# Performance work log

Measured on AMD Instinct MI355X. Metric: run time of the kernel, lower is better.

## Reference

```python
import jax, jax.numpy as jnp
import numpy as np

B, T, F_IN = 32, 2000, 1024
GROUPS, NUM_VARS, VQ_DIM = 2, 320, 256
VAR_DIM = VQ_DIM // GROUPS  # 128
TAU = 2.0  # curr_temp = max_temp at step 0
EPS = 1e-7


def setup_inputs() -> dict:
    key = jax.random.key(0)
    k1, k2, k3, k4 = jax.random.split(key, 4)
    x = jax.random.normal(k1, (B, T, F_IN), jnp.float32)
    # nn.Linear: weight ~ N(0,1) per module init, bias zeros
    proj_w = jax.random.normal(k2, (GROUPS * NUM_VARS, F_IN), jnp.float32)
    proj_b = jnp.zeros((GROUPS * NUM_VARS,), jnp.float32)
    # nn.init.uniform_ on vars (leading singleton dim dropped)
    codebook = jax.random.uniform(k3, (GROUPS * NUM_VARS, VAR_DIM), jnp.float32)
    # pre-sampled standard Gumbel noise (training-path gumbel_softmax)
    u = jax.random.uniform(k4, (B * T, GROUPS * NUM_VARS), jnp.float32, 1e-6, 1.0 - 1e-6)
    gumbel = -jnp.log(-jnp.log(u))
    return {"x": x, "proj_w": proj_w, "proj_b": proj_b, "codebook": codebook, "gumbel": gumbel}


def reference(x, proj_w, proj_b, codebook, gumbel):
    bsz, tsz, fsz = x.shape
    bt = bsz * tsz
    logits = x.reshape(bt, fsz) @ proj_w.T + proj_b                 # [BT, G*V]
    lg = logits.reshape(bt, GROUPS, NUM_VARS)                       # [BT, G, V]

    # hard codes (argmax of raw logits) -> code perplexity
    k = jnp.argmax(lg, axis=-1)                                     # [BT, G]
    hard_x = jax.nn.one_hot(k, NUM_VARS, dtype=lg.dtype)            # [BT, G, V]
    hard_probs = hard_x.mean(axis=0)                                # [G, V]
    code_perplexity = jnp.exp(-jnp.sum(hard_probs * jnp.log(hard_probs + EPS), -1)).sum()

    avg_probs = jax.nn.softmax(lg, axis=-1).mean(axis=0)            # [G, V]
    prob_perplex = jnp.exp(-jnp.sum(avg_probs * jnp.log(avg_probs + EPS), -1)).sum()

    # training path: gumbel_softmax(tau, hard=True) with straight-through
    g = gumbel.reshape(bt, GROUPS, NUM_VARS)
    y_soft = jax.nn.softmax((lg + g) / TAU, axis=-1)                # [BT, G, V]
    y_hard = jax.nn.one_hot(jnp.argmax(y_soft, -1), NUM_VARS, dtype=y_soft.dtype)
    y = y_hard + y_soft - jax.lax.stop_gradient(y_soft)             # straight-through

    # codebook weighted sum; original does (one_hot[...,None] * vars).sum over V
    cb = codebook.reshape(GROUPS, NUM_VARS, VAR_DIM)
    q = jnp.einsum("tgv,gvd->tgd", y, cb)                           # [BT, G, var_dim]
    q = q.reshape(bsz, tsz, VQ_DIM)
    return q, code_perplexity, prob_perplex
```

## Files before the change

kernel.cpp:

```cpp
#include <hip/hip_runtime.h>
#include <cstdint>
#include <cstddef>

#define BT_TOT 64000
#define FIN    1024
#define GV     640
#define NV     320
#define VD     128
#define INV_BT (1.0f/64000.0f)

#define ITER_B  81920
#define BUF_B   40960

typedef __attribute__((ext_vector_type(8))) __bf16 bf16x8;
typedef __attribute__((ext_vector_type(16))) float f32x16;

typedef __attribute__((address_space(1))) void gvoid_t;
typedef __attribute__((address_space(3))) void lvoid_t;

__device__ inline short f2bf(float x) {
    unsigned int u = __float_as_uint(x);
    unsigned int r = (u + 0x7fffu + ((u >> 16) & 1u)) >> 16;
    return (short)r;
}
__device__ inline float bf2f(short h) {
    return __uint_as_float(((unsigned int)(unsigned short)h) << 16);
}
__device__ inline bf16x8 ld_frag(const char* p) {
    union { uint4 u; bf16x8 v; } t;
    t.u = *(const uint4*)p;
    return t.v;
}
__device__ __forceinline__ void glds16(const void* g, void* l) {
    __builtin_amdgcn_global_load_lds((gvoid_t*)g, (lvoid_t*)l, 16, 0, 0);
}
__device__ __forceinline__ void cvt8(const float4 f0, const float4 f1,
                                     bf16x8& hh, bf16x8& ll) {
    union { float4 f[2]; float s[8]; } ua; ua.f[0] = f0; ua.f[1] = f1;
    union { short s[8]; bf16x8 v; } uh, ul;
#pragma unroll
    for (int e = 0; e < 8; ++e) {
        const short hb = f2bf(ua.s[e]);
        uh.s[e] = hb;
        ul.s[e] = f2bf(ua.s[e] - bf2f(hb));
    }
    hh = uh.v; ll = ul.v;
}

__global__ __launch_bounds__(256) void prep(
    const float* __restrict__ W, char* __restrict__ Wpk,
    float* __restrict__ psum_g, int* __restrict__ cnt_g)
{
    const int t = blockIdx.x * 256 + threadIdx.x;
    if (t < GV) { psum_g[t] = 0.f; cnt_g[t] = 0; }
    const int r    = t >> 7;
    const int ck8  = t & 127;
    const int iter = ck8 >> 2;
    const int c    = (ck8 >> 1) & 1;
    const int ch   = ck8 & 1;
    const int g    = (r >= NV) ? 1 : 0;
    const int cv   = r - g * NV;
    const float* src = W + (size_t)r * FIN + (size_t)ck8 * 8;
    const float4 a = ((const float4*)src)[0];
    const float4 b = ((const float4*)src)[1];
    float xs[8] = {a.x, a.y, a.z, a.w, b.x, b.y, b.z, b.w};
    short hi[8], lo[8];
#pragma unroll
    for (int e = 0; e < 8; ++e) {
        hi[e] = f2bf(xs[e]);
        lo[e] = f2bf(xs[e] - bf2f(hi[e]));
    }
    char* dst = Wpk + (size_t)iter * ITER_B + (size_t)g * BUF_B + (size_t)c * 20480
                    + (size_t)(cv * 32 + ch * 16);
    *(uint4*)dst           = *(uint4*)hi;
    *(uint4*)(dst + 10240) = *(uint4*)lo;
}

__global__ __launch_bounds__(512) void fused(
    const float* __restrict__ X, const char* __restrict__ Wpk,
    const float* __restrict__ bias, const float* __restrict__ gumbel,
    const float* __restrict__ codebook, float* __restrict__ q,
    float* __restrict__ psum_g, int* __restrict__ cnt_g)
{
    __shared__ __align__(16) char smem[2 * BUF_B];

    const int id = blockIdx.x;
    const int linear = (id & 7) * 64 + (id >> 3);
    if (linear >= 500) return;
    const int rb = linear >> 1, g = linear & 1;

    const int tid  = threadIdx.x;
    const int lane = tid & 63, wave = tid >> 6;
    const int cl = lane & 31, h = lane >> 5;
    const int row0 = rb * 256;
    const int arow = wave * 32 + cl;
    const int rdo  = cl * 32 + h * 16;

    f32x16 acc[10];
#pragma unroll
    for (int nt = 0; nt < 10; ++nt) acc[nt] = (f32x16)0.0f;

    const float* aptr  = X + (size_t)(row0 + arow) * FIN + h * 8;
    const char*  wbase = Wpk + (size_t)g * BUF_B;

    float4 xa0, xa1, xa2, xa3;
    {
#pragma unroll
        for (int j = 0; j < 5; ++j)
            glds16(wbase + (size_t)(tid + 512 * j) * 16, smem + (tid + 512 * j) * 16);
        __builtin_amdgcn_sched_barrier(0);
        xa0 = *(const float4*)(aptr);
        xa1 = *(const float4*)(aptr + 4);
        xa2 = *(const float4*)(aptr + 16);
        xa3 = *(const float4*)(aptr + 20);
        asm volatile("s_waitcnt vmcnt(4)" ::: "memory");
        __builtin_amdgcn_s_barrier();
    }

    for (int i = 0; i < 32; ++i) {
        const char* bufc = smem + (i & 1) * BUF_B;
        char* bufn = smem + ((i + 1) & 1) * BUF_B;
        const char* wsrc = wbase + (size_t)(i + 1) * ITER_B;
        const float* apn = aptr + (i + 1) * 32;
        const bool more = (i < 31);
        bf16x8 bh[5], bl[5], ah, al;

#pragma unroll
        for (int n = 0; n < 5; ++n) {
            bh[n] = ld_frag(bufc + n * 1024 + rdo);
            bl[n] = ld_frag(bufc + 10240 + n * 1024 + rdo);
        }
        if (more) {
            glds16(wsrc + (size_t)tid * 16,         bufn + tid * 16);
            glds16(wsrc + (size_t)(tid + 512) * 16, bufn + (tid + 512) * 16);
        }
        cvt8(xa0, xa1, ah, al);
        __builtin_amdgcn_sched_barrier(0);
        __builtin_amdgcn_s_barrier();
        asm volatile("s_waitcnt lgkmcnt(0)" ::: "memory");
        __builtin_amdgcn_sched_barrier(0);
        __builtin_amdgcn_s_setprio(1);
#pragma unroll
        for (int n = 0; n < 5; ++n) {
            acc[n] = __builtin_amdgcn_mfma_f32_32x32x16_bf16(ah, bh[n], acc[n], 0, 0, 0);
            acc[n] = __builtin_amdgcn_mfma_f32_32x32x16_bf16(al, bh[n], acc[n], 0, 0, 0);
            acc[n] = __builtin_amdgcn_mfma_f32_32x32x16_bf16(ah, bl[n], acc[n], 0, 0, 0);
        }
        __builtin_amdgcn_s_setprio(0);
        __builtin_amdgcn_s_barrier();

#pragma unroll
        for (int n = 0; n < 5; ++n) {
            bh[n] = ld_frag(bufc + (n + 5) * 1024 + rdo);
            bl[n] = ld_frag(bufc + 10240 + (n + 5) * 1024 + rdo);
        }
        if (more)
            glds16(wsrc + (size_t)(tid + 1024) * 16, bufn + (tid + 1024) * 16);
        __builtin_amdgcn_sched_barrier(0);
        __builtin_amdgcn_s_barrier();
        asm volatile("s_waitcnt lgkmcnt(0)" ::: "memory");
        __builtin_amdgcn_sched_barrier(0);
        __builtin_amdgcn_s_setprio(1);
#pragma unroll
        for (int n = 0; n < 5; ++n) {
            acc[n + 5] = __builtin_amdgcn_mfma_f32_32x32x16_bf16(ah, bh[n], acc[n + 5], 0, 0, 0);
            acc[n + 5] = __builtin_amdgcn_mfma_f32_32x32x16_bf16(al, bh[n], acc[n + 5], 0, 0, 0);
            acc[n + 5] = __builtin_amdgcn_mfma_f32_32x32x16_bf16(ah, bl[n], acc[n + 5], 0, 0, 0);
        }
        __builtin_amdgcn_s_setprio(0);
        __builtin_amdgcn_s_barrier();

#pragma unroll
        for (int n = 0; n < 5; ++n) {
            bh[n] = ld_frag(bufc + 20480 + n * 1024 + rdo);
            bl[n] = ld_frag(bufc + 30720 + n * 1024 + rdo);
        }
        if (more) {
            glds16(wsrc + (size_t)(tid + 1536) * 16, bufn + (tid + 1536) * 16);
            __builtin_amdgcn_sched_barrier(0);
            xa0 = *(const float4*)(apn);
            xa1 = *(const float4*)(apn + 4);
        }
        cvt8(xa2, xa3, ah, al);
        __builtin_amdgcn_sched_barrier(0);
        __builtin_amdgcn_s_barrier();
        asm volatile("s_waitcnt lgkmcnt(0)" ::: "memory");
        __builtin_amdgcn_sched_barrier(0);
        __builtin_amdgcn_s_setprio(1);
#pragma unroll
        for (int n = 0; n < 5; ++n) {
            acc[n] = __builtin_amdgcn_mfma_f32_32x32x16_bf16(ah, bh[n], acc[n], 0, 0, 0);
            acc[n] = __builtin_amdgcn_mfma_f32_32x32x16_bf16(al, bh[n], acc[n], 0, 0, 0);
            acc[n] = __builtin_amdgcn_mfma_f32_32x32x16_bf16(ah, bl[n], acc[n], 0, 0, 0);
        }
        __builtin_amdgcn_s_setprio(0);
        __builtin_amdgcn_s_barrier();

#pragma unroll
        for (int n = 0; n < 5; ++n) {
            bh[n] = ld_frag(bufc + 20480 + (n + 5) * 1024 + rdo);
            bl[n] = ld_frag(bufc + 30720 + (n + 5) * 1024 + rdo);
        }
        if (more) {
            glds16(wsrc + (size_t)(tid + 2048) * 16, bufn + (tid + 2048) * 16);
            __builtin_amdgcn_sched_barrier(0);
            xa2 = *(const float4*)(apn + 16);
            xa3 = *(const float4*)(apn + 20);
        }
        __builtin_amdgcn_sched_barrier(0);
        __builtin_amdgcn_s_barrier();
        asm volatile("s_waitcnt lgkmcnt(0)" ::: "memory");
        __builtin_amdgcn_sched_barrier(0);
        __builtin_amdgcn_s_setprio(1);
#pragma unroll
        for (int n = 0; n < 5; ++n) {
            acc[n + 5] = __builtin_amdgcn_mfma_f32_32x32x16_bf16(ah, bh[n], acc[n + 5], 0, 0, 0);
            acc[n + 5] = __builtin_amdgcn_mfma_f32_32x32x16_bf16(al, bh[n], acc[n + 5], 0, 0, 0);
            acc[n + 5] = __builtin_amdgcn_mfma_f32_32x32x16_bf16(ah, bl[n], acc[n + 5], 0, 0, 0);
        }
        __builtin_amdgcn_s_setprio(0);
        asm volatile("s_waitcnt vmcnt(2)" ::: "memory");
        __builtin_amdgcn_s_barrier();
    }

    float* psum_l = (float*)(smem);
    int*   cnt_l  = (int*)(smem + 1280);
    int*   gidx   = (int*)(smem + 2560);

    for (int i = tid; i < NV; i += 512) { psum_l[i] = 0.f; cnt_l[i] = 0; }
    __syncthreads();

#pragma unroll
    for (int nt = 0; nt < 10; ++nt) {
        const float bv = bias[g * NV + nt * 32 + cl];
#pragma unroll
        for (int r = 0; r < 16; ++r) acc[nt][r] += bv;
    }

    float pcol[10];
#pragma unroll
    for (int nt = 0; nt < 10; ++nt) pcol[nt] = 0.f;

#pragma unroll
    for (int reg = 0; reg < 16; ++reg) {
        const int rloc = wave * 32 + (reg & 3) + 8 * (reg >> 2) + 4 * h;
        const float* gp = gumbel + (size_t)(row0 + rloc) * GV + g * NV;
        float bestv = -3.4e38f, gbv = -3.4e38f;
        int bestc = 0, gbc = 0;
#pragma unroll
        for (int nt = 0; nt < 10; ++nt) {
            const float v = acc[nt][reg];
            const int cc = nt * 32 + cl;
            const float tv = v + gp[cc];
            if (v > bestv) { bestv = v; bestc = cc; }
            if (tv > gbv)  { gbv = tv;  gbc = cc; }
        }
#pragma unroll
        for (int off = 1; off < 32; off <<= 1) {
            const float v2 = __shfl_xor(bestv, off); const int c2 = __shfl_xor(bestc, off);
            if (v2 > bestv || (v2 == bestv && c2 < bestc)) { bestv = v2; bestc = c2; }
            const float g2 = __shfl_xor(gbv, off); const int gc2 = __shfl_xor(gbc, off);
            if (g2 > gbv || (g2 == gbv && gc2 < gbc)) { gbv = g2; gbc = gc2; }
        }
        float e[10], s = 0.f;
#pragma unroll
        for (int nt = 0; nt < 10; ++nt) { e[nt] = __expf(acc[nt][reg] - bestv); s += e[nt]; }
#pragma unroll
        for (int off = 1; off < 32; off <<= 1) s += __shfl_xor(s, off);
        const float inv_s = 1.0f / s;
#pragma unroll
        for (int nt = 0; nt < 10; ++nt) pcol[nt] += e[nt] * inv_s;
        if (cl == 0) {
            atomicAdd(&cnt_l[bestc], 1);
            gidx[rloc] = gbc;
        }
    }
#pragma unroll
    for (int nt = 0; nt < 10; ++nt) {
        const float v = pcol[nt] + __shfl_xor(pcol[nt], 32);
        if (h == 0) atomicAdd(&psum_l[nt * 32 + cl], v);
    }
    __syncthreads();

    {
        const int row = tid >> 1, half = tid & 1;
        const int idx = g * NV + gidx[row];
        const float4* srcp = (const float4*)(codebook + (size_t)idx * VD + half * 64);
        float4* dstp = (float4*)(q + (size_t)(row0 + row) * 256 + g * VD + half * 64);
#pragma unroll
        for (int i = 0; i < 16; ++i) dstp[i] = srcp[i];
    }
    for (int i = tid; i < NV; i += 512) {
        atomicAdd(&psum_g[g * NV + i], psum_l[i]);
        atomicAdd(&cnt_g[g * NV + i], cnt_l[i]);
    }
}

__global__ void finalize(const int* __restrict__ cnt_g, const float* __restrict__ psum_g,
                         float* __restrict__ out_scalars)
{
    const int lane = threadIdx.x;
    float hsum[2] = {0.f, 0.f}, p[2] = {0.f, 0.f};
    for (int i = lane; i < GV; i += 64) {
        const int g = i / NV;
        const float hp = (float)cnt_g[i] * INV_BT;
        const float ap = psum_g[i] * INV_BT;
        hsum[g] -= hp * logf(hp + 1e-7f);
        p[g]    -= ap * logf(ap + 1e-7f);
    }
#pragma unroll
    for (int off = 32; off > 0; off >>= 1) {
        hsum[0] += __shfl_xor(hsum[0], off); hsum[1] += __shfl_xor(hsum[1], off);
        p[0] += __shfl_xor(p[0], off);       p[1] += __shfl_xor(p[1], off);
    }
    if (lane == 0) {
        out_scalars[0] = expf(hsum[0]) + expf(hsum[1]);
        out_scalars[1] = expf(p[0]) + expf(p[1]);
    }
}

extern "C" void kernel_launch(void* const* d_in, const int* in_sizes, int n_in,
                              void* d_out, int out_size, void* d_ws, size_t ws_size,
                              hipStream_t stream)
{
    const float* X  = (const float*)d_in[0];
    const float* W  = (const float*)d_in[1];
    const float* Bv = (const float*)d_in[2];
    const float* CB = (const float*)d_in[3];
    const float* GU = (const float*)d_in[4];

    float* q = (float*)d_out;
    float* out_scalars = (float*)d_out + (size_t)BT_TOT * 256;

    char* ws = (char*)d_ws;
    float* psum_g = (float*)ws;
    int*   cnt_g  = (int*)(ws + 4096);
    char*  Wpk    = ws + 8192;

    prep<<<320, 256, 0, stream>>>(W, Wpk, psum_g, cnt_g);
    fused<<<512, 512, 0, stream>>>(X, Wpk, Bv, GU, CB, q, psum_g, cnt_g);
    finalize<<<1, 64, 0, stream>>>(cnt_g, psum_g, out_scalars);
}
```

Measured before the change: 664.1 us.

## Retile GEMM waves to 2x2 row/column split with single-barrier K pipeline

Each wave now computes 64 rows by 160 columns (two M tiles by five N tiles) instead of 32 rows by all 320 columns. Each B fragment read from LDS is therefore reused across two A tiles, which cuts LDS traffic per MFMA. The per-iteration schedule is reduced from four barrier phases to one wait and barrier, with the whole next weight chunk and the next X values prefetched up front. Because a row's columns are now split across two waves, the epilogue combines argmax, Gumbel argmax and softmax sums through shared memory, which adds extra syncs and raises register pressure from the doubled X prefetch buffers.

```diff
diff --git a/kernel.cpp b/kernel.cpp
--- a/kernel.cpp
+++ b/kernel.cpp
@@ -91,194 +91,219 @@
 
     const int tid  = threadIdx.x;
     const int lane = tid & 63, wave = tid >> 6;
+    const int rs = wave >> 1, cs = wave & 1;
     const int cl = lane & 31, h = lane >> 5;
     const int row0 = rb * 256;
-    const int arow = wave * 32 + cl;
-    const int rdo  = cl * 32 + h * 16;
-
-    f32x16 acc[10];
-#pragma unroll
-    for (int nt = 0; nt < 10; ++nt) acc[nt] = (f32x16)0.0f;
-
-    const float* aptr  = X + (size_t)(row0 + arow) * FIN + h * 8;
+    const int bofs = cs * 5120 + cl * 32 + h * 16;
+
+    f32x16 acc[2][5];
+#pragma unroll
+    for (int mt = 0; mt < 2; ++mt)
+#pragma unroll
+        for (int nt = 0; nt < 5; ++nt) acc[mt][nt] = (f32x16)0.0f;
+
+    const float* ap0 = X + (size_t)(row0 + rs * 64 + cl) * FIN + h * 8;
+    const float* ap1 = ap0 + (size_t)32 * FIN;
     const char*  wbase = Wpk + (size_t)g * BUF_B;
 
-    float4 xa0, xa1, xa2, xa3;
+    float4 xa_c0[2][2], xa_c1[2][2], xn_c0[2][2], xn_c1[2][2];
+
     {
 #pragma unroll
         for (int j = 0; j < 5; ++j)
             glds16(wbase + (size_t)(tid + 512 * j) * 16, smem + (tid + 512 * j) * 16);
         __builtin_amdgcn_sched_barrier(0);
-        xa0 = *(const float4*)(aptr);
-        xa1 = *(const float4*)(aptr + 4);
-        xa2 = *(const float4*)(aptr + 16);
-        xa3 = *(const float4*)(aptr + 20);
-        asm volatile("s_waitcnt vmcnt(4)" ::: "memory");
+        xa_c0[0][0] = *(const float4*)(ap0);      xa_c0[0][1] = *(const float4*)(ap0 + 4);
+        xa_c0[1][0] = *(const float4*)(ap1);      xa_c0[1][1] = *(const float4*)(ap1 + 4);
+        xa_c1[0][0] = *(const float4*)(ap0 + 16); xa_c1[0][1] = *(const float4*)(ap0 + 20);
+        xa_c1[1][0] = *(const float4*)(ap1 + 16); xa_c1[1][1] = *(const float4*)(ap1 + 20);
+    }
+
+    for (int i = 0; i < 32; ++i) {
+        asm volatile("s_waitcnt vmcnt(8)" ::: "memory");
         __builtin_amdgcn_s_barrier();
-    }
-
-    for (int i = 0; i < 32; ++i) {
+        __builtin_amdgcn_sched_barrier(0);
+
         const char* bufc = smem + (i & 1) * BUF_B;
         char* bufn = smem + ((i + 1) & 1) * BUF_B;
         const char* wsrc = wbase + (size_t)(i + 1) * ITER_B;
-        const float* apn = aptr + (i + 1) * 32;
         const bool more = (i < 31);
-        bf16x8 bh[5], bl[5], ah, al;
-
-#pragma unroll
-        for (int n = 0; n < 5; ++n) {
-            bh[n] = ld_frag(bufc + n * 1024 + rdo);
-            bl[n] = ld_frag(bufc + 10240 + n * 1024 + rdo);
-        }
+
         if (more) {
-            glds16(wsrc + (size_t)tid * 16,         bufn + tid * 16);
-            glds16(wsrc + (size_t)(tid + 512) * 16, bufn + (tid + 512) * 16);
-        }
-        cvt8(xa0, xa1, ah, al);
+#pragma unroll
+            for (int j = 0; j < 5; ++j)
+                glds16(wsrc + (size_t)(tid + 512 * j) * 16, bufn + (tid + 512 * j) * 16);
+            __builtin_amdgcn_sched_barrier(0);
+            const float* n0 = ap0 + (i + 1) * 32;
+            const float* n1 = ap1 + (i + 1) * 32;
+            xn_c0[0][0] = *(const float4*)(n0);  xn_c0[0][1] = *(const float4*)(n0 + 4);
+            xn_c0[1][0] = *(const float4*)(n1);  xn_c0[1][1] = *(const float4*)(n1 + 4);
+            __builtin_amdgcn_sched_barrier(0);
+        }
+
+        bf16x8 bh[5], bl[5], ah[2], al[2];
+#pragma unroll
+        for (int n = 0; n < 5; ++n) {
+            bh[n] = ld_frag(bufc + n * 1024 + bofs);
+            bl[n] = ld_frag(bufc + 10240 + n * 1024 + bofs);
+        }
+        cvt8(xa_c0[0][0], xa_c0[0][1], ah[0], al[0]);
+        cvt8(xa_c0[1][0], xa_c0[1][1], ah[1], al[1]);
+        __builtin_amdgcn_s_setprio(1);
+#pragma unroll
+        for (int n = 0; n < 5; ++n) {
+            acc[0][n] = __builtin_amdgcn_mfma_f32_32x32x16_bf16(ah[0], bh[n], acc[0][n], 0, 0, 0);
+            acc[1][n] = __builtin_amdgcn_mfma_f32_32x32x16_bf16(ah[1], bh[n], acc[1][n], 0, 0, 0);
+        }
+#pragma unroll
+        for (int n = 0; n < 5; ++n) {
+            acc[0][n] = __builtin_amdgcn_mfma_f32_32x32x16_bf16(al[0], bh[n], acc[0][n], 0, 0, 0);
+            acc[1][n] = __builtin_amdgcn_mfma_f32_32x32x16_bf16(al[1], bh[n], acc[1][n], 0, 0, 0);
+        }
+#pragma unroll
+        for (int n = 0; n < 5; ++n) {
+            acc[0][n] = __builtin_amdgcn_mfma_f32_32x32x16_bf16(ah[0], bl[n], acc[0][n], 0, 0, 0);
+            acc[1][n] = __builtin_amdgcn_mfma_f32_32x32x16_bf16(ah[1], bl[n], acc[1][n], 0, 0, 0);
+        }
+        __builtin_amdgcn_s_setprio(0);
         __builtin_amdgcn_sched_barrier(0);
-        __builtin_amdgcn_s_barrier();
-        asm volatile("s_waitcnt lgkmcnt(0)" ::: "memory");
-        __builtin_amdgcn_sched_barrier(0);
+
+#pragma unroll
+        for (int n = 0; n < 5; ++n) {
+            bh[n] = ld_frag(bufc + 20480 + n * 1024 + bofs);
+            bl[n] = ld_frag(bufc + 30720 + n * 1024 + bofs);
+        }
+        cvt8(xa_c1[0][0], xa_c1[0][1], ah[0], al[0]);
+        cvt8(xa_c1[1][0], xa_c1[1][1], ah[1], al[1]);
+        if (more) {
+            const float* n0 = ap0 + (i + 1) * 32;
+            const float* n1 = ap1 + (i + 1) * 32;
+            xn_c1[0][0] = *(const float4*)(n0 + 16); xn_c1[0][1] = *(const float4*)(n0 + 20);
+            xn_c1[1][0] = *(const float4*)(n1 + 16); xn_c1[1][1] = *(const float4*)(n1 + 20);
+        }
         __builtin_amdgcn_s_setprio(1);
 #pragma unroll
         for (int n = 0; n < 5; ++n) {
-            acc[n] = __builtin_amdgcn_mfma_f32_32x32x16_bf16(ah, bh[n], acc[n], 0, 0, 0);
-            acc[n] = __builtin_amdgcn_mfma_f32_32x32x16_bf16(al, bh[n], acc[n], 0, 0, 0);
-            acc[n] = __builtin_amdgcn_mfma_f32_32x32x16_bf16(ah, bl[n], acc[n], 0, 0, 0);
+            acc[0][n] = __builtin_amdgcn_mfma_f32_32x32x16_bf16(ah[0], bh[n], acc[0][n], 0, 0, 0);
+            acc[1][n] = __builtin_amdgcn_mfma_f32_32x32x16_bf16(ah[1], bh[n], acc[1][n], 0, 0, 0);
+        }
+#pragma unroll
+        for (int n = 0; n < 5; ++n) {
+            acc[0][n] = __builtin_amdgcn_mfma_f32_32x32x16_bf16(al[0], bh[n], acc[0][n], 0, 0, 0);
+            acc[1][n] = __builtin_amdgcn_mfma_f32_32x32x16_bf16(al[1], bh[n], acc[1][n], 0, 0, 0);
+        }
+#pragma unroll
+        for (int n = 0; n < 5; ++n) {
+            acc[0][n] = __builtin_amdgcn_mfma_f32_32x32x16_bf16(ah[0], bl[n], acc[0][n], 0, 0, 0);
+            acc[1][n] = __builtin_amdgcn_mfma_f32_32x32x16_bf16(ah[1], bl[n], acc[1][n], 0, 0, 0);
         }
         __builtin_amdgcn_s_setprio(0);
-        __builtin_amdgcn_s_barrier();
-
-#pragma unroll
-        for (int n = 0; n < 5; ++n) {
-            bh[n] = ld_frag(bufc + (n + 5) * 1024 + rdo);
-            bl[n] = ld_frag(bufc + 10240 + (n + 5) * 1024 + rdo);
-        }
-        if (more)
-            glds16(wsrc + (size_t)(tid + 1024) * 16, bufn + (tid + 1024) * 16);
-        __builtin_amdgcn_sched_barrier(0);
-        __builtin_amdgcn_s_barrier();
-        asm volatile("s_waitcnt lgkmcnt(0)" ::: "memory");
-        __builtin_amdgcn_sched_barrier(0);
-        __builtin_amdgcn_s_setprio(1);
-#pragma unroll
-        for (int n = 0; n < 5; ++n) {
-            acc[n + 5] = __builtin_amdgcn_mfma_f32_32x32x16_bf16(ah, bh[n], acc[n + 5], 0, 0, 0);
-            acc[n + 5] = __builtin_amdgcn_mfma_f32_32x32x16_bf16(al, bh[n], acc[n + 5], 0, 0, 0);
-            acc[n + 5] = __builtin_amdgcn_mfma_f32_32x32x16_bf16(ah, bl[n], acc[n + 5], 0, 0, 0);
-        }
-        __builtin_amdgcn_s_setprio(0);
-        __builtin_amdgcn_s_barrier();
-
-#pragma unroll
-        for (int n = 0; n < 5; ++n) {
-            bh[n] = ld_frag(bufc + 20480 + n * 1024 + rdo);
-            bl[n] = ld_frag(bufc + 30720 + n * 1024 + rdo);
-        }
-        if (more) {
-            glds16(wsrc + (size_t)(tid + 1536) * 16, bufn + (tid + 1536) * 16);
-            __builtin_amdgcn_sched_barrier(0);
-            xa0 = *(const float4*)(apn);
-            xa1 = *(const float4*)(apn + 4);
-        }
-        cvt8(xa2, xa3, ah, al);
-        __builtin_amdgcn_sched_barrier(0);
-        __builtin_amdgcn_s_barrier();
-        asm volatile("s_waitcnt lgkmcnt(0)" ::: "memory");
-        __builtin_amdgcn_sched_barrier(0);
-        __builtin_amdgcn_s_setprio(1);
-#pragma unroll
-        for (int n = 0; n < 5; ++n) {
-            acc[n] = __builtin_amdgcn_mfma_f32_32x32x16_bf16(ah, bh[n], acc[n], 0, 0, 0);
-            acc[n] = __builtin_amdgcn_mfma_f32_32x32x16_bf16(al, bh[n], acc[n], 0, 0, 0);
-            acc[n] = __builtin_amdgcn_mfma_f32_32x32x16_bf16(ah, bl[n], acc[n], 0, 0, 0);
-        }
-        __builtin_amdgcn_s_setprio(0);
-        __builtin_amdgcn_s_barrier();
-
-#pragma unroll
-        for (int n = 0; n < 5; ++n) {
-            bh[n] = ld_frag(bufc + 20480 + (n + 5) * 1024 + rdo);
-            bl[n] = ld_frag(bufc + 30720 + (n + 5) * 1024 + rdo);
-        }
-        if (more) {
-            glds16(wsrc + (size_t)(tid + 2048) * 16, bufn + (tid + 2048) * 16);
-            __builtin_amdgcn_sched_barrier(0);
-            xa2 = *(const float4*)(apn + 16);
-            xa3 = *(const float4*)(apn + 20);
-        }
-        __builtin_amdgcn_sched_barrier(0);
-        __builtin_amdgcn_s_barrier();
-        asm volatile("s_waitcnt lgkmcnt(0)" ::: "memory");
-        __builtin_amdgcn_sched_barrier(0);
-        __builtin_amdgcn_s_setprio(1);
-#pragma unroll
-        for (int n = 0; n < 5; ++n) {
-            acc[n + 5] = __builtin_amdgcn_mfma_f32_32x32x16_bf16(ah, bh[n], acc[n + 5], 0, 0, 0);
-            acc[n + 5] = __builtin_amdgcn_mfma_f32_32x32x16_bf16(al, bh[n], acc[n + 5], 0, 0, 0);
-            acc[n + 5] = __builtin_amdgcn_mfma_f32_32x32x16_bf16(ah, bl[n], acc[n + 5], 0, 0, 0);
-        }
-        __builtin_amdgcn_s_setprio(0);
-        asm volatile("s_waitcnt vmcnt(2)" ::: "memory");
-        __builtin_amdgcn_s_barrier();
+
+#pragma unroll
+        for (int mt = 0; mt < 2; ++mt)
+#pragma unroll
+            for (int hf = 0; hf < 2; ++hf) {
+                xa_c0[mt][hf] = xn_c0[mt][hf];
+                xa_c1[mt][hf] = xn_c1[mt][hf];
+            }
     }
 
     float* psum_l = (float*)(smem);
     int*   cnt_l  = (int*)(smem + 1280);
     int*   gidx   = (int*)(smem + 2560);
-
+    float* sv  = (float*)(smem + 4096);
+    int*   sc  = (int*)(smem + 6144);
+    float* sgv = (float*)(smem + 8192);
+    int*   sgc = (int*)(smem + 10240);
+    float* ss  = (float*)(smem + 12288);
+
+    __syncthreads();
     for (int i = tid; i < NV; i += 512) { psum_l[i] = 0.f; cnt_l[i] = 0; }
     __syncthreads();
 
 #pragma unroll
-    for (int nt = 0; nt < 10; ++nt) {
-        const float bv = bias[g * NV + nt * 32 + cl];
-#pragma unroll
-        for (int r = 0; r < 16; ++r) acc[nt][r] += bv;
-    }
-
-    float pcol[10];
-#pragma unroll
-    for (int nt = 0; nt < 10; ++nt) pcol[nt] = 0.f;
-
-#pragma unroll
-    for (int reg = 0; reg < 16; ++reg) {
-        const int rloc = wave * 32 + (reg & 3) + 8 * (reg >> 2) + 4 * h;
-        const float* gp = gumbel + (size_t)(row0 + rloc) * GV + g * NV;
-        float bestv = -3.4e38f, gbv = -3.4e38f;
-        int bestc = 0, gbc = 0;
-#pragma unroll
-        for (int nt = 0; nt < 10; ++nt) {
-            const float v = acc[nt][reg];
-            const int cc = nt * 32 + cl;
-            const float tv = v + gp[cc];
-            if (v > bestv) { bestv = v; bestc = cc; }
-            if (tv > gbv)  { gbv = tv;  gbc = cc; }
-        }
-#pragma unroll
-        for (int off = 1; off < 32; off <<= 1) {
-            const float v2 = __shfl_xor(bestv, off); const int c2 = __shfl_xor(bestc, off);
-            if (v2 > bestv || (v2 == bestv && c2 < bestc)) { bestv = v2; bestc = c2; }
-            const float g2 = __shfl_xor(gbv, off); const int gc2 = __shfl_xor(gbc, off);
-            if (g2 > gbv || (g2 == gbv && gc2 < gbc)) { gbv = g2; gbc = gc2; }
-        }
-        float e[10], s = 0.f;
-#pragma unroll
-        for (int nt = 0; nt < 10; ++nt) { e[nt] = __expf(acc[nt][reg] - bestv); s += e[nt]; }
-#pragma unroll
-        for (int off = 1; off < 32; off <<= 1) s += __shfl_xor(s, off);
-        const float inv_s = 1.0f / s;
-#pragma unroll
-        for (int nt = 0; nt < 10; ++nt) pcol[nt] += e[nt] * inv_s;
-        if (cl == 0) {
-            atomicAdd(&cnt_l[bestc], 1);
-            gidx[rloc] = gbc;
-        }
-    }
-#pragma unroll
-    for (int nt = 0; nt < 10; ++nt) {
+    for (int nt = 0; nt < 5; ++nt) {
+        const float bv = bias[g * NV + cs * 160 + nt * 32 + cl];
+#pragma unroll
+        for (int mt = 0; mt < 2; ++mt)
+#pragma unroll
+            for (int r = 0; r < 16; ++r) acc[mt][nt][r] += bv;
+    }
+
+    float pcol[5];
+#pragma unroll
+    for (int nt = 0; nt < 5; ++nt) pcol[nt] = 0.f;
+
+#pragma unroll
+    for (int mt = 0; mt < 2; ++mt) {
+#pragma unroll
+        for (int c0 = 0; c0 < 16; c0 += 4) {
+            float bvv[4], gvv[4], sll[4];
+            int bcc[4], gcc[4];
+#pragma unroll
+            for (int j = 0; j < 4; ++j) {
+                const int reg = c0 + j;
+                const int rloc = rs * 64 + mt * 32 + (reg & 3) + 8 * (reg >> 2) + 4 * h;
+                const float* gp = gumbel + (size_t)(row0 + rloc) * GV + g * NV;
+                float bestv = -3.4e38f, gbv = -3.4e38f;
+                int bestc = 0, gbc = 0;
+#pragma unroll
+                for (int nt = 0; nt < 5; ++nt) {
+                    const float v = acc[mt][nt][reg];
+                    const int cc = cs * 160 + nt * 32 + cl;
+                    const float tv = v + gp[cc];
+                    if (v > bestv) { bestv = v; bestc = cc; }
+                    if (tv > gbv)  { gbv = tv;  gbc = cc; }
+                }
+#pragma unroll
+                for (int off = 1; off < 32; off <<= 1) {
+                    const float v2 = __shfl_xor(bestv, off); const int c2 = __shfl_xor(bestc, off);
+                    if (v2 > bestv || (v2 == bestv && c2 < bestc)) { bestv = v2; bestc = c2; }
+                    const float g2 = __shfl_xor(gbv, off); const int gc2 = __shfl_xor(gbc, off);
+                    if (g2 > gbv || (g2 == gbv && gc2 < gbc)) { gbv = g2; gbc = gc2; }
+                }
+                float s = 0.f;
+#pragma unroll
+                for (int nt = 0; nt < 5; ++nt) s += __expf(acc[mt][nt][reg] - bestv);
+#pragma unroll
+                for (int off = 1; off < 32; off <<= 1) s += __shfl_xor(s, off);
+                bvv[j] = bestv; bcc[j] = bestc; gvv[j] = gbv; gcc[j] = gbc; sll[j] = s;
+                if (cl == 0) {
+                    const int si = rloc * 2 + cs;
+                    sv[si] = bestv; sc[si] = bestc; sgv[si] = gbv; sgc[si] = gbc; ss[si] = s;
+                }
+            }
+            __syncthreads();
+#pragma unroll
+            for (int j = 0; j < 4; ++j) {
+                const int reg = c0 + j;
+                const int rloc = rs * 64 + mt * 32 + (reg & 3) + 8 * (reg >> 2) + 4 * h;
+                const int pi = rloc * 2 + (cs ^ 1);
+                const float pv = sv[pi]; const int pc = sc[pi];
+                const float pgv = sgv[pi]; const int pgc = sgc[pi];
+                const float ps = ss[pi];
+                float m = bvv[j]; int mc = bcc[j];
+                if (pv > m || (pv == m && pc < mc)) { m = pv; mc = pc; }
+                float mg = gvv[j]; int mgc = gcc[j];
+                if (pgv > mg || (pgv == mg && pgc < mgc)) { mg = pgv; mgc = pgc; }
+                const float fl = __expf(bvv[j] - m);
+                const float stot = sll[j] * fl + ps * __expf(pv - m);
+                const float fscale = fl / stot;
+#pragma unroll
+                for (int nt = 0; nt < 5; ++nt)
+                    pcol[nt] += __expf(acc[mt][nt][reg] - bvv[j]) * fscale;
+                if (cs == 0 && cl == 0) {
+                    atomicAdd(&cnt_l[mc], 1);
+                    gidx[rloc] = mgc;
+                }
+            }
+        }
+    }
+
+#pragma unroll
+    for (int nt = 0; nt < 5; ++nt) {
         const float v = pcol[nt] + __shfl_xor(pcol[nt], 32);
-        if (h == 0) atomicAdd(&psum_l[nt * 32 + cl], v);
+        if (h == 0) atomicAdd(&psum_l[cs * 160 + nt * 32 + cl], v);
     }
     __syncthreads();
 
```

Result: slower. 1.740 ms (+162.0%).
